# Optimization experiments

Hardware: AMD Instinct MI355X
Metric: run time of the kernel (lower is better)

## Reference

```python
import jax, jax.numpy as jnp
import numpy as np

B, N, D, H, C = 2, 2048, 1024, 16, 3
Dh = D // H


def setup_inputs() -> dict:
    key = jax.random.key(0)
    ks = jax.random.split(key, 6)
    x = jax.random.normal(ks[0], (B, N, D), jnp.float32)
    coords = jax.random.normal(ks[1], (B, N, C), jnp.float32)
    attn_mask = jax.random.normal(ks[2], (N, N), jnp.float32) * 0.1  # additive float bias (2d kind)
    Wqkv = jax.random.normal(ks[3], (D, 3 * D), jnp.float32) / np.sqrt(D)
    bqkv = jax.random.normal(ks[4], (3 * D,), jnp.float32) * 0.01
    rel_weight = jax.random.normal(ks[5], (H, C), jnp.float32) * 0.02
    return {"x": x, "coords": coords, "attn_mask": attn_mask,
            "Wqkv": Wqkv, "bqkv": bqkv, "rel_weight": rel_weight}


def reference(x, coords, attn_mask, Wqkv, bqkv, rel_weight):
    b, n, d = x.shape
    h, dh = rel_weight.shape[0], d // rel_weight.shape[0]
    scale = 1.0 / np.sqrt(float(dh))

    qkv = x @ Wqkv + bqkv                      # [B,N,3D]
    q, k, v = jnp.split(qkv, 3, axis=-1)

    def to_heads(t):
        return t.reshape(b, n, h, dh).transpose(0, 2, 1, 3)  # [B,H,N,Dh]

    qh, kh, vh = to_heads(q), to_heads(k), to_heads(v)

    # scaled dot-product scores (flex_attention applies scale before score_mod)
    scores = jnp.einsum('bhnd,bhmd->bhnm', qh, kh) * scale   # [B,H,N,N]

    # coordinate-derived per-head relative bias: coord_proj[b,h,qi] - coord_proj[b,h,kj]
    coord_proj = jnp.einsum('bnc,hc->bhn', coords.astype(jnp.float32), rel_weight)
    scores = scores + coord_proj[:, :, :, None] - coord_proj[:, :, None, :]

    # additive float mask bias, '2d' kind: shape (N,N) broadcast over B,H
    scores = scores + attn_mask[None, None, :, :]

    attn = jax.nn.softmax(scores, axis=-1)
    out = jnp.einsum('bhnm,bhmd->bhnd', attn, vh)            # [B,H,N,Dh]
    return out.transpose(0, 2, 1, 3).reshape(b, n, d)        # [B,N,D]
```

## Files before the change

kernel.cpp:

```cpp
#include <hip/hip_runtime.h>

typedef _Float16 half8 __attribute__((ext_vector_type(8)));
typedef _Float16 half4 __attribute__((ext_vector_type(4)));
typedef _Float16 half2v __attribute__((ext_vector_type(2)));
typedef float floatx4 __attribute__((ext_vector_type(4)));

#define LOG2E 1.44269504088896f
#define QSCALE 0.18033688011112f

__device__ __forceinline__ void async16(const void* g, void* l) {
    __builtin_amdgcn_global_load_lds(
        (const __attribute__((address_space(1))) unsigned int*)g,
        (__attribute__((address_space(3))) unsigned int*)l, 16, 0, 0);
}
__device__ __forceinline__ half4 pack4(float a, float b, float c, float d) {
    half2v lo = __builtin_bit_cast(half2v, __builtin_amdgcn_cvt_pkrtz(a, b));
    half2v hi = __builtin_bit_cast(half2v, __builtin_amdgcn_cvt_pkrtz(c, d));
    half4 r; r[0] = lo[0]; r[1] = lo[1]; r[2] = hi[0]; r[3] = hi[1];
    return r;
}

__global__ __launch_bounds__(256) void k_prep(
    const float* __restrict__ x, const float* __restrict__ W,
    const float* __restrict__ coords, const float* __restrict__ rw,
    const float* __restrict__ mask,
    _Float16* __restrict__ xh, _Float16* __restrict__ Wt,
    float* __restrict__ negcp, _Float16* __restrict__ maskp) {
    __shared__ float smem[4352];
    int bx = blockIdx.x, tid = threadIdx.x;
    if (bx < 2048) {
        int i = bx * 256 + tid;
        const floatx4* xin = (const floatx4*)x;
        floatx4 a = xin[i * 2];
        floatx4 b = xin[i * 2 + 1];
        half8 h;
        h[0] = (_Float16)a[0]; h[1] = (_Float16)a[1]; h[2] = (_Float16)a[2]; h[3] = (_Float16)a[3];
        h[4] = (_Float16)b[0]; h[5] = (_Float16)b[1]; h[6] = (_Float16)b[2]; h[7] = (_Float16)b[3];
        *(half8*)&xh[i * 8] = h;
    } else if (bx < 5120) {
        int b2 = bx - 2048;
        int n0 = (b2 % 96) * 32, k0 = (b2 / 96) * 32;
        int tx = tid & 31, ty = tid >> 5;
        float (*tile)[33] = (float(*)[33])smem;
        #pragma unroll
        for (int r = 0; r < 4; ++r)
            tile[ty + r * 8][tx] = W[(size_t)(k0 + ty + r * 8) * 3072 + n0 + tx];
        __syncthreads();
        #pragma unroll
        for (int r = 0; r < 4; ++r)
            Wt[(size_t)(n0 + ty + r * 8) * 1024 + k0 + tx] = (_Float16)tile[tx][ty + r * 8];
    } else if (bx < 5376) {
        int idx = (bx - 5120) * 256 + tid;
        int bh = idx >> 11, n = idx & 2047;
        int b = bh >> 4, h = bh & 15;
        const float* c = &coords[(b * 2048 + n) * 3];
        const float* w = &rw[h * 3];
        negcp[idx] = -LOG2E * (c[0] * w[0] + c[1] * w[1] + c[2] * w[2]);
    } else {
        int bid = bx - 5376;
        int qt = bid >> 5, kt = bid & 31;
        int row0 = qt * 64, col0 = kt * 64;
        int lr = tid >> 2, lc = (tid & 3) * 16;
        #pragma unroll
        for (int j = 0; j < 4; ++j)
            *(floatx4*)&smem[lr * 68 + lc + j * 4] =
                *(const floatx4*)&mask[(size_t)(row0 + lr) * 2048 + col0 + lc + j * 4];
        __syncthreads();
        int w = tid >> 6, lane = tid & 63, quad = lane >> 4, l16 = lane & 15;
        half4* outp = (half4*)maskp + (size_t)((qt * 32 + kt) * 4 + w) * 256 + lane;
        #pragma unroll
        for (int t = 0; t < 4; ++t) {
            floatx4 m = *(const floatx4*)&smem[(w * 16 + l16) * 68 + t * 16 + quad * 4];
            outp[t * 64] = pack4(m[0] * LOG2E, m[1] * LOG2E, m[2] * LOG2E, m[3] * LOG2E);
        }
    }
}

__global__ __launch_bounds__(256) void k_gemm(
    const _Float16* __restrict__ Ah, const _Float16* __restrict__ Bt,
    const float* __restrict__ bias,
    _Float16* __restrict__ qh, _Float16* __restrict__ kh, _Float16* __restrict__ vt) {
    __shared__ _Float16 smem[16384];
    int tid = threadIdx.x;
    int w = tid >> 6, lane = tid & 63;
    int quad = lane >> 4, l16 = lane & 15;
    int m0 = blockIdx.y * 128;
    int n0 = blockIdx.x * 128;
    bool QK = n0 < 2048;
    int mq = (w >> 1) * 64, nq = (w & 1) * 64;
    int c0 = n0 + nq;

    int rl4 = lane >> 2;
    int pb4 = lane & 3;
    floatx4 acc[4][4] = {};

    const _Float16* ap[2];
    const _Float16* bp[2];
    #pragma unroll
    for (int j = 0; j < 2; ++j) {
        int row = w * 32 + j * 16 + rl4;
        int lb = pb4 ^ (row & 3) ^ ((row >> 2) & 3);
        ap[j] = Ah + (size_t)(m0 + row) * 1024 + lb * 8;
        bp[j] = Bt + (size_t)(n0 + row) * 1024 + lb * 8;
    }

    #define GSTAGE(buf) {                                      \
        _Float16* As_ = smem + (buf) * 8192;                   \
        _Float16* Bs_ = As_ + 4096;                            \
        async16(ap[0], &As_[(w * 32) * 32]);                   \
        async16(ap[1], &As_[(w * 32 + 16) * 32]);              \
        async16(bp[0], &Bs_[(w * 32) * 32]);                   \
        async16(bp[1], &Bs_[(w * 32 + 16) * 32]);              \
        ap[0] += 32; ap[1] += 32; bp[0] += 32; bp[1] += 32;    \
    }

    #define GBODY(cur, last) {                                                         \
        __syncthreads();                                                               \
        if (!(last)) GSTAGE((cur) ^ 1);                                                \
        const _Float16* As_ = smem + (cur) * 8192;                                     \
        const _Float16* Bs_ = As_ + 4096;                                              \
        half8 af[4], bf[4];                                                            \
        _Pragma("unroll")                                                              \
        for (int s = 0; s < 4; ++s) {                                                  \
            int ra = mq + s * 16 + l16;                                                \
            af[s] = *(const half8*)&As_[ra * 32 +                                      \
                ((quad ^ (ra & 3) ^ ((ra >> 2) & 3)) << 3)];                           \
            int rb = nq + s * 16 + l16;                                                \
            bf[s] = *(const half8*)&Bs_[rb * 32 +                                      \
                ((quad ^ (rb & 3) ^ ((rb >> 2) & 3)) << 3)];                           \
        }                                                                              \
        if (QK) {                                                                      \
            _Pragma("unroll")                                                          \
            for (int ms = 0; ms < 4; ++ms)                                             \
                _Pragma("unroll")                                                      \
                for (int ns = 0; ns < 4; ++ns)                                         \
                    acc[ms][ns] = __builtin_amdgcn_mfma_f32_16x16x32_f16(              \
                        bf[ns], af[ms], acc[ms][ns], 0, 0, 0);                         \
        } else {                                                                       \
            _Pragma("unroll")                                                          \
            for (int ms = 0; ms < 4; ++ms)                                             \
                _Pragma("unroll")                                                      \
                for (int ns = 0; ns < 4; ++ns)                                         \
                    acc[ms][ns] = __builtin_amdgcn_mfma_f32_16x16x32_f16(              \
                        af[ms], bf[ns], acc[ms][ns], 0, 0, 0);                         \
        }                                                                              \
    }

    GSTAGE(0);
    #pragma unroll 1
    for (int kt2 = 0; kt2 < 15; ++kt2) {
        GBODY(0, false);
        GBODY(1, false);
    }
    GBODY(0, false);
    GBODY(1, true);
    #undef GBODY
    #undef GSTAGE

    __syncthreads();

    _Float16* Ls = smem + w * 2304;
    int rl = lane >> 3, pb = lane & 7;
    int b = (m0 + mq) >> 11, nbase = (m0 + mq) & 2047;
    if (QK) {
        float qsc = (c0 < 1024) ? QSCALE : 1.0f;
        int h2 = c0 >> 6;
        _Float16* dst = (h2 < 16 ? qh : kh) + (size_t)(((b << 4) + (h2 & 15)) * 2048) * 64;
        int d0 = pb << 3;
        #pragma unroll
        for (int p = 0; p < 2; ++p) {
            #pragma unroll
            for (int ns = 0; ns < 4; ++ns) {
                floatx4 b4 = *(const floatx4*)&bias[c0 + ns * 16 + quad * 4];
                #pragma unroll
                for (int m2 = 0; m2 < 2; ++m2) {
                    int ms = p * 2 + m2;
                    floatx4 v;
                    #pragma unroll
                    for (int i = 0; i < 4; ++i) v[i] = (acc[ms][ns][i] + b4[i]) * qsc;
                    *(half4*)&Ls[(m2 * 16 + l16) * 72 + ns * 16 + quad * 4] =
                        pack4(v[0], v[1], v[2], v[3]);
                }
            }
            #pragma unroll
            for (int rep = 0; rep < 4; ++rep) {
                int nl = rep * 8 + rl;
                half8 v = *(const half8*)&Ls[nl * 72 + d0];
                *(half8*)&dst[(size_t)(nbase + p * 32 + nl) * 64 + d0] = v;
            }
        }
    } else {
        int h = (c0 - 2048) >> 6;
        _Float16* dst = vt + (size_t)(((b << 4) + h) * 64) * 2048;
        int noff = pb << 3;
        #pragma unroll
        for (int p = 0; p < 2; ++p) {
            #pragma unroll
            for (int n2 = 0; n2 < 2; ++n2) {
                int ns = p * 2 + n2;
                float bv = bias[c0 + ns * 16 + l16];
                #pragma unroll
                for (int ms = 0; ms < 4; ++ms) {
                    *(half4*)&Ls[(n2 * 16 + l16) * 72 + ms * 16 + quad * 4] =
                        pack4(acc[ms][ns][0] + bv, acc[ms][ns][1] + bv,
                              acc[ms][ns][2] + bv, acc[ms][ns][3] + bv);
                }
            }
            #pragma unroll
            for (int rep = 0; rep < 4; ++rep) {
                int cl = rep * 8 + rl;
                half8 v = *(const half8*)&Ls[cl * 72 + noff];
                *(half8*)&dst[(size_t)(p * 32 + cl) * 2048 + nbase + noff] = v;
            }
        }
    }
}

__global__ __launch_bounds__(256) void k_attn(
    const _Float16* __restrict__ qh, const _Float16* __restrict__ kh,
    const _Float16* __restrict__ vt, const _Float16* __restrict__ maskp,
    const float* __restrict__ negcp, float* __restrict__ out) {
    __shared__ _Float16 KV[2][8192];
    int tid = threadIdx.x;
    int w = tid >> 6, lane = tid & 63;
    int quad = lane >> 4, l16 = lane & 15;
    int rl = lane >> 3, pb = lane & 7;
    int bid = blockIdx.x;
    int qt = bid & 31, bh = bid >> 5;
    int b = bh >> 4, h = bh & 15;
    int qrow = qt * 64 + w * 16;

    half8 qf[2];
    {
        const _Float16* qp = &qh[((size_t)bh * 2048 + qrow + l16) * 64];
        qf[0] = *(const half8*)&qp[quad * 8];
        qf[1] = *(const half8*)&qp[32 + quad * 8];
    }
    floatx4 o[4] = {};
    floatx4 ol = {};
    half4 ones;
    ones[0] = (_Float16)1.f; ones[1] = (_Float16)1.f;
    ones[2] = (_Float16)1.f; ones[3] = (_Float16)1.f;

    int sw = (pb ^ rl) << 3;
    const _Float16* kp0 = kh + (size_t)bh * 131072 + (size_t)(w * 16 + rl) * 64 + sw;
    const _Float16* kp1 = kp0 + 512;
    const _Float16* vp0 = vt + (size_t)bh * 131072 + (size_t)(w * 16 + rl) * 2048 + sw;
    const _Float16* vp1 = vp0 + 16384;
    const half4* mp = (const half4*)maskp + (size_t)(qt * 128 + w) * 256 + lane;
    const float* ncpp = negcp + bh * 2048 + quad * 4;

    #define STAGE(buf) {                                             \
        async16(kp0, &KV[buf][(w * 16) * 64]);                       \
        async16(kp1, &KV[buf][(w * 16 + 8) * 64]);                   \
        async16(vp0, &KV[buf][4096 + (w * 16) * 64]);                \
        async16(vp1, &KV[buf][4096 + (w * 16 + 8) * 64]);            \
        kp0 += 4096; kp1 += 4096; vp0 += 64; vp1 += 64;              \
    }

    #define BODY(cur, last) {                                                          \
        __syncthreads();                                                               \
        if (!(last)) STAGE((cur) ^ 1);                                                 \
        half4 mload[4];                                                                \
        floatx4 ncv[4];                                                                \
        _Pragma("unroll")                                                              \
        for (int t = 0; t < 4; ++t) mload[t] = mp[t * 64];                             \
        _Pragma("unroll")                                                              \
        for (int t = 0; t < 4; ++t) ncv[t] = *(const floatx4*)&ncpp[t * 16];           \
        mp += 1024; ncpp += 64;                                                        \
        floatx4 ci[4];                                                                 \
        _Pragma("unroll")                                                              \
        for (int t = 0; t < 4; ++t)                                                    \
            _Pragma("unroll")                                                          \
            for (int i = 0; i < 4; ++i)                                                \
                ci[t][i] = (float)mload[t][i] + ncv[t][i];                             \
        const _Float16* Ksc = &KV[cur][0];                                             \
        const _Float16* Vsc = &KV[cur][4096];                                          \
        floatx4 st[4];                                                                 \
        _Pragma("unroll")                                                              \
        for (int t = 0; t < 4; ++t) {                                                  \
            int r = t * 16 + l16;                                                      \
            half8 k0 = *(const half8*)&Ksc[r * 64 + ((quad ^ (r & 7)) << 3)];          \
            half8 k1 = *(const half8*)&Ksc[r * 64 + (((quad + 4) ^ (r & 7)) << 3)];    \
            floatx4 z = ci[t];                                                         \
            z = __builtin_amdgcn_mfma_f32_16x16x32_f16(k0, qf[0], z, 0, 0, 0);         \
            z = __builtin_amdgcn_mfma_f32_16x16x32_f16(k1, qf[1], z, 0, 0, 0);         \
            st[t] = z;                                                                 \
        }                                                                              \
        half4 pt[4];                                                                   \
        _Pragma("unroll")                                                              \
        for (int t = 0; t < 4; ++t) {                                                  \
            float p0 = __builtin_amdgcn_exp2f(st[t][0]);                               \
            float p1 = __builtin_amdgcn_exp2f(st[t][1]);                               \
            float p2 = __builtin_amdgcn_exp2f(st[t][2]);                               \
            float p3 = __builtin_amdgcn_exp2f(st[t][3]);                               \
            pt[t] = pack4(p0, p1, p2, p3);                                             \
        }                                                                              \
        _Pragma("unroll")                                                              \
        for (int t = 0; t < 4; ++t)                                                    \
            ol = __builtin_amdgcn_mfma_f32_16x16x16f16(ones, pt[t], ol, 0, 0, 0);      \
        _Pragma("unroll")                                                              \
        for (int dt = 0; dt < 4; ++dt) {                                               \
            int rv = dt * 16 + l16;                                                    \
            _Pragma("unroll")                                                          \
            for (int t = 0; t < 4; ++t) {                                              \
                half4 vf = *(const half4*)&Vsc[rv * 64 +                               \
                    (((t * 2 + (quad >> 1)) ^ (rv & 7)) << 3) + ((quad & 1) << 2)];    \
                o[dt] = __builtin_amdgcn_mfma_f32_16x16x16f16(vf, pt[t], o[dt], 0, 0, 0); \
            }                                                                          \
        }                                                                              \
    }

    STAGE(0);
    #pragma unroll 1
    for (int kt2 = 0; kt2 < 15; ++kt2) {
        BODY(0, false);
        BODY(1, false);
    }
    BODY(0, false);
    BODY(1, true);
    #undef BODY
    #undef STAGE

    float inv = 1.f / ol[0];
    #pragma unroll
    for (int dt = 0; dt < 4; ++dt) {
        floatx4 r;
        #pragma unroll
        for (int i = 0; i < 4; ++i) r[i] = o[dt][i] * inv;
        *(floatx4*)&out[((size_t)(b * 2048 + qrow + l16)) * 1024 + h * 64 + dt * 16 + quad * 4] = r;
    }
}

extern "C" void kernel_launch(void* const* d_in, const int* in_sizes, int n_in,
                              void* d_out, int out_size, void* d_ws, size_t ws_size,
                              hipStream_t stream) {
    const float* x      = (const float*)d_in[0];
    const float* coords = (const float*)d_in[1];
    const float* mask   = (const float*)d_in[2];
    const float* Wqkv   = (const float*)d_in[3];
    const float* bqkv   = (const float*)d_in[4];
    const float* rw     = (const float*)d_in[5];
    float* out = (float*)d_out;

    char* ws = (char*)d_ws;
    _Float16* xh    = (_Float16*)(ws);
    _Float16* maskp = (_Float16*)(ws + 8388608);
    _Float16* Wt    = (_Float16*)(ws + 16777216);
    _Float16* qh    = (_Float16*)(ws + 23068672);
    _Float16* kh    = (_Float16*)(ws + 31457280);
    _Float16* vt    = (_Float16*)(ws + 39845888);
    float*    ncp   = (float*)(ws + 48234496);

    k_prep<<<6400, 256, 0, stream>>>(x, Wqkv, coords, rw, mask, xh, Wt, ncp, maskp);
    k_gemm<<<dim3(24, 32), 256, 0, stream>>>(xh, Wt, bqkv, qh, kh, vt);
    k_attn<<<1024, 256, 0, stream>>>(qh, kh, vt, maskp, ncp, out);
}
```

Baseline: 197.9 us.

## Fold key coord bias into V as exp factor and process two query groups per wave

The per-key coordinate bias exp(-cp_k) is precomputed in fp16 and multiplied into V during the QKV GEMM epilogue. The softmax denominator uses that factor as the ones-vector in the row-sum MFMA, which removes the per-element bias add from the attention inner loop. Each wave now handles 32 query rows (two 16-row groups) against the same staged K/V tiles, doubling K/V reuse, halving the grid and adding a launch_bounds occupancy hint. The cost is more registers per wave and fp16 precision limits on the exp factor, and the query-side bias is still dropped because it cancels in softmax.

```diff
diff --git a/kernel.cpp b/kernel.cpp
--- a/kernel.cpp
+++ b/kernel.cpp
@@ -25,7 +25,7 @@
     const float* __restrict__ coords, const float* __restrict__ rw,
     const float* __restrict__ mask,
     _Float16* __restrict__ xh, _Float16* __restrict__ Wt,
-    float* __restrict__ negcp, _Float16* __restrict__ maskp) {
+    _Float16* __restrict__ esch, _Float16* __restrict__ maskp) {
     __shared__ float smem[4352];
     int bx = blockIdx.x, tid = threadIdx.x;
     if (bx < 2048) {
@@ -55,7 +55,8 @@
         int b = bh >> 4, h = bh & 15;
         const float* c = &coords[(b * 2048 + n) * 3];
         const float* w = &rw[h * 3];
-        negcp[idx] = -LOG2E * (c[0] * w[0] + c[1] * w[1] + c[2] * w[2]);
+        float v = -LOG2E * (c[0] * w[0] + c[1] * w[1] + c[2] * w[2]);
+        esch[idx] = (_Float16)__builtin_amdgcn_exp2f(v);
     } else {
         int bid = bx - 5376;
         int qt = bid >> 5, kt = bid & 31;
@@ -78,7 +79,7 @@
 
 __global__ __launch_bounds__(256) void k_gemm(
     const _Float16* __restrict__ Ah, const _Float16* __restrict__ Bt,
-    const float* __restrict__ bias,
+    const float* __restrict__ bias, const _Float16* __restrict__ esch,
     _Float16* __restrict__ qh, _Float16* __restrict__ kh, _Float16* __restrict__ vt) {
     __shared__ _Float16 smem[16384];
     int tid = threadIdx.x;
@@ -192,6 +193,14 @@
     } else {
         int h = (c0 - 2048) >> 6;
         _Float16* dst = vt + (size_t)(((b << 4) + h) * 64) * 2048;
+        const _Float16* ePtr = esch + (size_t)((b << 4) + h) * 2048 + nbase + quad * 4;
+        float ef[4][4];
+        #pragma unroll
+        for (int ms = 0; ms < 4; ++ms) {
+            half4 e4 = *(const half4*)&ePtr[ms * 16];
+            #pragma unroll
+            for (int i = 0; i < 4; ++i) ef[ms][i] = (float)e4[i];
+        }
         int noff = pb << 3;
         #pragma unroll
         for (int p = 0; p < 2; ++p) {
@@ -202,8 +211,10 @@
                 #pragma unroll
                 for (int ms = 0; ms < 4; ++ms) {
                     *(half4*)&Ls[(n2 * 16 + l16) * 72 + ms * 16 + quad * 4] =
-                        pack4(acc[ms][ns][0] + bv, acc[ms][ns][1] + bv,
-                              acc[ms][ns][2] + bv, acc[ms][ns][3] + bv);
+                        pack4((acc[ms][ns][0] + bv) * ef[ms][0],
+                              (acc[ms][ns][1] + bv) * ef[ms][1],
+                              (acc[ms][ns][2] + bv) * ef[ms][2],
+                              (acc[ms][ns][3] + bv) * ef[ms][3]);
                 }
             }
             #pragma unroll
@@ -216,39 +227,39 @@
     }
 }
 
-__global__ __launch_bounds__(256) void k_attn(
+__global__ __launch_bounds__(256, 2) void k_attn(
     const _Float16* __restrict__ qh, const _Float16* __restrict__ kh,
     const _Float16* __restrict__ vt, const _Float16* __restrict__ maskp,
-    const float* __restrict__ negcp, float* __restrict__ out) {
+    const _Float16* __restrict__ esch, float* __restrict__ out) {
     __shared__ _Float16 KV[2][8192];
     int tid = threadIdx.x;
     int w = tid >> 6, lane = tid & 63;
     int quad = lane >> 4, l16 = lane & 15;
     int rl = lane >> 3, pb = lane & 7;
     int bid = blockIdx.x;
-    int qt = bid & 31, bh = bid >> 5;
+    int qt2 = bid & 15, bh = bid >> 4;
     int b = bh >> 4, h = bh & 15;
-    int qrow = qt * 64 + w * 16;
-
-    half8 qf[2];
-    {
-        const _Float16* qp = &qh[((size_t)bh * 2048 + qrow + l16) * 64];
-        qf[0] = *(const half8*)&qp[quad * 8];
-        qf[1] = *(const half8*)&qp[32 + quad * 8];
-    }
-    floatx4 o[4] = {};
-    floatx4 ol = {};
-    half4 ones;
-    ones[0] = (_Float16)1.f; ones[1] = (_Float16)1.f;
-    ones[2] = (_Float16)1.f; ones[3] = (_Float16)1.f;
+    int qrow = qt2 * 128 + w * 32;
+
+    half8 qf[2][2];
+    #pragma unroll
+    for (int g = 0; g < 2; ++g) {
+        const _Float16* qp = &qh[((size_t)bh * 2048 + qrow + g * 16 + l16) * 64];
+        qf[g][0] = *(const half8*)&qp[quad * 8];
+        qf[g][1] = *(const half8*)&qp[32 + quad * 8];
+    }
+    floatx4 o0[4] = {}, o1[4] = {};
+    floatx4 ol0 = {}, ol1 = {};
 
     int sw = (pb ^ rl) << 3;
     const _Float16* kp0 = kh + (size_t)bh * 131072 + (size_t)(w * 16 + rl) * 64 + sw;
     const _Float16* kp1 = kp0 + 512;
     const _Float16* vp0 = vt + (size_t)bh * 131072 + (size_t)(w * 16 + rl) * 2048 + sw;
     const _Float16* vp1 = vp0 + 16384;
-    const half4* mp = (const half4*)maskp + (size_t)(qt * 128 + w) * 256 + lane;
-    const float* ncpp = negcp + bh * 2048 + quad * 4;
+    const half4* mp0 = (const half4*)maskp +
+        ((size_t)(qt2 * 2 + (w >> 1)) * 128 + (w & 1) * 2) * 256 + lane;
+    const half4* mp1 = mp0 + 256;
+    const _Float16* ep = esch + bh * 2048 + quad * 4;
 
     #define STAGE(buf) {                                             \
         async16(kp0, &KV[buf][(w * 16) * 64]);                       \
@@ -261,44 +272,46 @@
     #define BODY(cur, last) {                                                          \
         __syncthreads();                                                               \
         if (!(last)) STAGE((cur) ^ 1);                                                 \
-        half4 mload[4];                                                                \
-        floatx4 ncv[4];                                                                \
-        _Pragma("unroll")                                                              \
-        for (int t = 0; t < 4; ++t) mload[t] = mp[t * 64];                             \
-        _Pragma("unroll")                                                              \
-        for (int t = 0; t < 4; ++t) ncv[t] = *(const floatx4*)&ncpp[t * 16];           \
-        mp += 1024; ncpp += 64;                                                        \
-        floatx4 ci[4];                                                                 \
-        _Pragma("unroll")                                                              \
-        for (int t = 0; t < 4; ++t)                                                    \
-            _Pragma("unroll")                                                          \
-            for (int i = 0; i < 4; ++i)                                                \
-                ci[t][i] = (float)mload[t][i] + ncv[t][i];                             \
+        half4 mload[2][4];                                                             \
+        half4 ev[4];                                                                   \
+        _Pragma("unroll")                                                              \
+        for (int t = 0; t < 4; ++t) mload[0][t] = mp0[t * 64];                         \
+        _Pragma("unroll")                                                              \
+        for (int t = 0; t < 4; ++t) mload[1][t] = mp1[t * 64];                         \
+        _Pragma("unroll")                                                              \
+        for (int t = 0; t < 4; ++t) ev[t] = *(const half4*)&ep[t * 16];                \
+        mp0 += 1024; mp1 += 1024; ep += 64;                                            \
         const _Float16* Ksc = &KV[cur][0];                                             \
         const _Float16* Vsc = &KV[cur][4096];                                          \
-        floatx4 st[4];                                                                 \
+        half8 kf0[4], kf1[4];                                                          \
         _Pragma("unroll")                                                              \
         for (int t = 0; t < 4; ++t) {                                                  \
             int r = t * 16 + l16;                                                      \
-            half8 k0 = *(const half8*)&Ksc[r * 64 + ((quad ^ (r & 7)) << 3)];          \
-            half8 k1 = *(const half8*)&Ksc[r * 64 + (((quad + 4) ^ (r & 7)) << 3)];    \
-            floatx4 z = ci[t];                                                         \
-            z = __builtin_amdgcn_mfma_f32_16x16x32_f16(k0, qf[0], z, 0, 0, 0);         \
-            z = __builtin_amdgcn_mfma_f32_16x16x32_f16(k1, qf[1], z, 0, 0, 0);         \
-            st[t] = z;                                                                 \
-        }                                                                              \
-        half4 pt[4];                                                                   \
+            kf0[t] = *(const half8*)&Ksc[r * 64 + ((quad ^ (r & 7)) << 3)];            \
+            kf1[t] = *(const half8*)&Ksc[r * 64 + (((quad + 4) ^ (r & 7)) << 3)];      \
+        }                                                                              \
+        half4 pt[2][4];                                                                \
+        _Pragma("unroll")                                                              \
+        for (int g = 0; g < 2; ++g) {                                                  \
+            _Pragma("unroll")                                                          \
+            for (int t = 0; t < 4; ++t) {                                              \
+                half4 ml = mload[g][t];                                                \
+                floatx4 z;                                                             \
+                z[0] = (float)ml[0]; z[1] = (float)ml[1];                              \
+                z[2] = (float)ml[2]; z[3] = (float)ml[3];                              \
+                z = __builtin_amdgcn_mfma_f32_16x16x32_f16(kf0[t], qf[g][0], z, 0, 0, 0); \
+                z = __builtin_amdgcn_mfma_f32_16x16x32_f16(kf1[t], qf[g][1], z, 0, 0, 0); \
+                pt[g][t] = pack4(__builtin_amdgcn_exp2f(z[0]),                         \
+                                 __builtin_amdgcn_exp2f(z[1]),                         \
+                                 __builtin_amdgcn_exp2f(z[2]),                         \
+                                 __builtin_amdgcn_exp2f(z[3]));                        \
+            }                                                                          \
+        }                                                                              \
         _Pragma("unroll")                                                              \
         for (int t = 0; t < 4; ++t) {                                                  \
-            float p0 = __builtin_amdgcn_exp2f(st[t][0]);                               \
-            float p1 = __builtin_amdgcn_exp2f(st[t][1]);                               \
-            float p2 = __builtin_amdgcn_exp2f(st[t][2]);                               \
-            float p3 = __builtin_amdgcn_exp2f(st[t][3]);                               \
-            pt[t] = pack4(p0, p1, p2, p3);                                             \
-        }                                                                              \
-        _Pragma("unroll")                                                              \
-        for (int t = 0; t < 4; ++t)                                                    \
-            ol = __builtin_amdgcn_mfma_f32_16x16x16f16(ones, pt[t], ol, 0, 0, 0);      \
+            ol0 = __builtin_amdgcn_mfma_f32_16x16x16f16(ev[t], pt[0][t], ol0, 0, 0, 0); \
+            ol1 = __builtin_amdgcn_mfma_f32_16x16x16f16(ev[t], pt[1][t], ol1, 0, 0, 0); \
+        }                                                                              \
         _Pragma("unroll")                                                              \
         for (int dt = 0; dt < 4; ++dt) {                                               \
             int rv = dt * 16 + l16;                                                    \
@@ -306,7 +319,8 @@
             for (int t = 0; t < 4; ++t) {                                              \
                 half4 vf = *(const half4*)&Vsc[rv * 64 +                               \
                     (((t * 2 + (quad >> 1)) ^ (rv & 7)) << 3) + ((quad & 1) << 2)];    \
-                o[dt] = __builtin_amdgcn_mfma_f32_16x16x16f16(vf, pt[t], o[dt], 0, 0, 0); \
+                o0[dt] = __builtin_amdgcn_mfma_f32_16x16x16f16(vf, pt[0][t], o0[dt], 0, 0, 0); \
+                o1[dt] = __builtin_amdgcn_mfma_f32_16x16x16f16(vf, pt[1][t], o1[dt], 0, 0, 0); \
             }                                                                          \
         }                                                                              \
     }
@@ -322,13 +336,16 @@
     #undef BODY
     #undef STAGE
 
-    float inv = 1.f / ol[0];
+    float inv0 = 1.f / ol0[0];
+    float inv1 = 1.f / ol1[0];
+    size_t obase = ((size_t)(b * 2048 + qrow + l16)) * 1024 + h * 64 + quad * 4;
     #pragma unroll
     for (int dt = 0; dt < 4; ++dt) {
-        floatx4 r;
-        #pragma unroll
-        for (int i = 0; i < 4; ++i) r[i] = o[dt][i] * inv;
-        *(floatx4*)&out[((size_t)(b * 2048 + qrow + l16)) * 1024 + h * 64 + dt * 16 + quad * 4] = r;
+        floatx4 r0, r1;
+        #pragma unroll
+        for (int i = 0; i < 4; ++i) { r0[i] = o0[dt][i] * inv0; r1[i] = o1[dt][i] * inv1; }
+        *(floatx4*)&out[obase + dt * 16] = r0;
+        *(floatx4*)&out[obase + (size_t)16 * 1024 + dt * 16] = r1;
     }
 }
 
@@ -350,9 +367,9 @@
     _Float16* qh    = (_Float16*)(ws + 23068672);
     _Float16* kh    = (_Float16*)(ws + 31457280);
     _Float16* vt    = (_Float16*)(ws + 39845888);
-    float*    ncp   = (float*)(ws + 48234496);
-
-    k_prep<<<6400, 256, 0, stream>>>(x, Wqkv, coords, rw, mask, xh, Wt, ncp, maskp);
-    k_gemm<<<dim3(24, 32), 256, 0, stream>>>(xh, Wt, bqkv, qh, kh, vt);
-    k_attn<<<1024, 256, 0, stream>>>(qh, kh, vt, maskp, ncp, out);
-}
+    _Float16* esch  = (_Float16*)(ws + 48234496);
+
+    k_prep<<<6400, 256, 0, stream>>>(x, Wqkv, coords, rw, mask, xh, Wt, esch, maskp);
+    k_gemm<<<dim3(24, 32), 256, 0, stream>>>(xh, Wt, bqkv, esch, qh, kh, vt);
+    k_attn<<<512, 256, 0, stream>>>(qh, kh, vt, maskp, esch, out);
+}
```

Measured after the change: 189.7 us. 4.1% less time.
